# Kernel optimization log

Measured on AMD Instinct MI355X. Metric: run time of the kernel, lower is better.

The kernel has to match this reference:

```python
import jax, jax.numpy as jnp
import numpy as np


def _proj(x, w, b):
    # 1x1 conv as channel matmul: x (n,c,h,w), w (k,c), b (k,) -> (n,k,h,w)
    return jnp.einsum('nchw,kc->nkhw', x, w) + b[None, :, None, None]


def setup_inputs() -> dict:
    key = jax.random.key(0)
    ks = jax.random.split(key, 9)
    cin, cinter = 256, 128
    n, h, w = 4, 64, 64
    s = lambda fan_in: 1.0 / np.sqrt(fan_in)
    return {
        'x': jax.random.normal(ks[0], (n, cin, h, w), jnp.float32),
        'theta_w': jax.random.normal(ks[1], (cinter, cin), jnp.float32) * s(cin),
        'theta_b': jax.random.normal(ks[2], (cinter,), jnp.float32) * 0.01,
        'phi_w': jax.random.normal(ks[3], (cinter, cin), jnp.float32) * s(cin),
        'phi_b': jax.random.normal(ks[4], (cinter,), jnp.float32) * 0.01,
        'g_w': jax.random.normal(ks[5], (cinter, cin), jnp.float32) * s(cin),
        'g_b': jax.random.normal(ks[6], (cinter,), jnp.float32) * 0.01,
        'w_w': jax.random.normal(ks[7], (cin, cinter), jnp.float32) * s(cinter),
        'w_b': jax.random.normal(ks[8], (cin,), jnp.float32) * 0.01,
    }


def reference(x, theta_w, theta_b, phi_w, phi_b, g_w, g_b, w_w, w_b):
    n, c, h, w = x.shape
    cinter = theta_w.shape[0]
    hw = h * w
    theta_x = _proj(x, theta_w, theta_b).reshape(n, cinter, hw)  # (n,ci,HW)
    phi_x = _proj(x, phi_w, phi_b).reshape(n, cinter, hw)        # (n,ci,HW)
    g_x = _proj(x, g_w, g_b).reshape(n, cinter, hw)              # (n,ci,HW)
    # f_x = phi^T @ theta : (n, HW, HW), softmax over last dim (theta positions)
    f_x = jnp.einsum('nci,ncj->nij', phi_x, theta_x)
    f_x = jax.nn.softmax(f_x, axis=-1)
    # attended = g @ f : (n, ci, HW)
    att = jnp.einsum('nci,nij->ncj', g_x, f_x).reshape(n, cinter, h, w)
    res_x = _proj(att, w_w, w_b)  # (n, c, h, w)
    return x + res_x
```

## Files before the change

### kernel.cpp

```cpp
#include <hip/hip_runtime.h>
#include <hip/hip_bf16.h>

#define B_ 4
#define C_ 256
#define CI_ 128
#define P_ 4096
#define LOG2E 1.44269504088896340736f

typedef __attribute__((ext_vector_type(8))) _Float16 half8;
typedef __attribute__((ext_vector_type(2))) __fp16 fp16x2;
typedef __attribute__((ext_vector_type(8))) short short8;
typedef __attribute__((ext_vector_type(4))) short short4v;
typedef __attribute__((ext_vector_type(4))) float floatx4;

__device__ __forceinline__ float bf2f(ushort h) {
  union { unsigned u; float f; } v; v.u = ((unsigned)h) << 16; return v.f;
}
__device__ __forceinline__ ushort f2bf(float f) {
  union { float f; unsigned u; } v; v.f = f;
  unsigned r = v.u + 0x7FFFu + ((v.u >> 16) & 1u);
  return (ushort)(r >> 16);
}
__device__ __forceinline__ ushort f2h(float f) {
  _Float16 h = (_Float16)f;
  union { _Float16 h; ushort u; } v; v.h = h; return v.u;
}
__device__ __forceinline__ uint2 pk4h(float a, float b, float c, float d) {
  union { fp16x2 h[2]; uint2 u; } pk;
  pk.h[0] = __builtin_amdgcn_cvt_pkrtz(a, b);
  pk.h[1] = __builtin_amdgcn_cvt_pkrtz(c, d);
  return pk.u;
}

#define MFMA16(a, b, c) __builtin_amdgcn_mfma_f32_16x16x32_f16((a), (b), (c), 0, 0, 0)

__device__ __forceinline__ int detect_bf16(const ushort* __restrict__ xu) {
  __shared__ int cnt_;
  if (threadIdx.x == 0) cnt_ = 0;
  __syncthreads();
  int local = 0;
  int t = threadIdx.x & 255;
#pragma unroll
  for (int s = 0; s < 8; ++s) {
    ushort u = xu[(t * 8 + s) * 2];
    int e = (u >> 7) & 0xFF;
    local += (e >= 0x70 && e <= 0x84) ? 1 : 0;
  }
  atomicAdd(&cnt_, local);
  __syncthreads();
  return cnt_ > 1024;
}

__global__ void k_trc(const void* __restrict__ xv, ushort* __restrict__ xT,
                      const void* __restrict__ s0, const void* __restrict__ s1,
                      const void* __restrict__ s2, const void* __restrict__ s3,
                      const void* __restrict__ tbv, const void* __restrict__ pbv,
                      const void* __restrict__ gbv, const void* __restrict__ wbv,
                      ushort* __restrict__ dstW, float* __restrict__ biasf) {
  int is_bf16 = detect_bf16((const ushort*)xv);
  int bid = blockIdx.x;
  int t = threadIdx.x;
  if (bid < 1024) {
    __shared__ __align__(16) ushort tile[64][74];
    int pb = (bid & 63) * 64;
    int cb = ((bid >> 6) & 3) * 64;
    int b = bid >> 8;
#pragma unroll
    for (int it = 0; it < 2; ++it) {
      int lin = it * 256 + t;
      int c = lin >> 3;
      int p = (lin & 7) * 8;
      size_t base = ((size_t)(b * C_) + cb + c) * P_ + pb + p;
      float vv[8];
      if (is_bf16) {
        short8 v = *(const short8*)((const ushort*)xv + base);
#pragma unroll
        for (int i = 0; i < 8; ++i) vv[i] = bf2f((ushort)v[i]);
      } else {
        const float* xf = (const float*)xv;
        float4 v0 = *(const float4*)(xf + base);
        float4 v1 = *(const float4*)(xf + base + 4);
        vv[0] = v0.x; vv[1] = v0.y; vv[2] = v0.z; vv[3] = v0.w;
        vv[4] = v1.x; vv[5] = v1.y; vv[6] = v1.z; vv[7] = v1.w;
      }
#pragma unroll
      for (int i = 0; i < 8; ++i) {
        int iw = (i + t) & 7;
        tile[p + iw][c] = f2h(vv[iw]);
      }
    }
    __syncthreads();
#pragma unroll
    for (int it = 0; it < 2; ++it) {
      int lin = it * 256 + t;
      int p = lin >> 3;
      int c = (lin & 7) * 8;
      short8 v = *(const short8*)&tile[p][c];
      *(short8*)(xT + ((size_t)(b * P_) + pb + p) * C_ + cb + c) = v;
    }
  } else if (bid < 1536) {
    int wid = bid - 1024;
    int a = wid >> 7;
    const void* srcs[4] = {s0, s1, s2, s3};
    int i = (wid & 127) * 256 + t;
    float v = is_bf16 ? bf2f(((const ushort*)srcs[a])[i]) : ((const float*)srcs[a])[i];
    dstW[a * 32768 + i] = f2h(v);
  } else {
    int idx = (bid - 1536) * 256 + t;
    if (idx < 640) {
      const void* src; int loc;
      if (idx < 128)      { src = tbv; loc = idx; }
      else if (idx < 256) { src = pbv; loc = idx - 128; }
      else if (idx < 384) { src = gbv; loc = idx - 256; }
      else                { src = wbv; loc = idx - 384; }
      float v = is_bf16 ? bf2f(((const ushort*)src)[loc]) : ((const float*)src)[loc];
      biasf[idx] = v;
    }
  }
}

__global__ __launch_bounds__(256, 4) void k_proj(
    const ushort* __restrict__ xT, const ushort* __restrict__ Wh,
    const float* __restrict__ biasf,
    ushort* __restrict__ thetaT, ushort* __restrict__ phiT,
    ushort* __restrict__ g) {
  int t = threadIdx.x;
  int w = t >> 6, lane = t & 63, l = lane & 15, q = lane >> 4;
  int pblk = blockIdx.x * 32;
  int b = blockIdx.y;
  floatx4 acc[2][6];
#pragma unroll
  for (int ps = 0; ps < 2; ++ps)
#pragma unroll
    for (int ks = 0; ks < 6; ++ks) acc[ps][ks] = (floatx4){0.f, 0.f, 0.f, 0.f};
  const ushort* xrow[2];
#pragma unroll
  for (int ps = 0; ps < 2; ++ps)
    xrow[ps] = xT + ((size_t)(b * P_) + pblk + ps * 16 + l) * C_;
  const ushort* wrow[6];
  int prj[6], kloc[6];
#pragma unroll
  for (int ks = 0; ks < 6; ++ks) {
    int kg = w * 96 + ks * 16;
    prj[ks] = kg >> 7;
    kloc[ks] = kg & 127;
    wrow[ks] = Wh + prj[ks] * 32768 + (size_t)(kloc[ks] + l) * C_;
  }
  for (int c = 0; c < C_; c += 32) {
    half8 av[2], wv[6];
#pragma unroll
    for (int ps = 0; ps < 2; ++ps) av[ps] = *(const half8*)(xrow[ps] + c + q * 8);
#pragma unroll
    for (int ks = 0; ks < 6; ++ks) wv[ks] = *(const half8*)(wrow[ks] + c + q * 8);
#pragma unroll
    for (int ps = 0; ps < 2; ++ps)
#pragma unroll
      for (int ks = 0; ks < 6; ++ks)
        acc[ps][ks] = MFMA16(av[ps], wv[ks], acc[ps][ks]);
  }
#pragma unroll
  for (int ks = 0; ks < 6; ++ks) {
    float bias = biasf[prj[ks] * 128 + kloc[ks] + l];
#pragma unroll
    for (int ps = 0; ps < 2; ++ps) {
      floatx4 d = acc[ps][ks];
      if (prj[ks] < 2) {
        ushort* dst = (prj[ks] == 0 ? thetaT : phiT) +
                      ((size_t)(b * P_) + pblk + ps * 16 + q * 4) * CI_ + kloc[ks] + l;
#pragma unroll
        for (int r = 0; r < 4; ++r) dst[(size_t)r * CI_] = f2h(d[r] + bias);
      } else {
        ushort* dst = g + ((size_t)(b * CI_) + kloc[ks] + l) * P_ + pblk + ps * 16 + q * 4;
        short4v pk;
#pragma unroll
        for (int r = 0; r < 4; ++r) pk[r] = (short)f2h(d[r] + bias);
        *(short4v*)dst = pk;
      }
    }
  }
}

__global__ __launch_bounds__(256, 2) void k_stats(
    const ushort* __restrict__ phiT, const ushort* __restrict__ thetaT,
    float* __restrict__ part) {
  int t = threadIdx.x, w = t >> 6, lane = t & 63, l = lane & 15, q = lane >> 4;
  int wgid = blockIdx.x;
  int xcd = wgid & 7, slot = wgid >> 3;
  int st = xcd + 8 * (slot >> 4);
  int i0 = (slot & 15) * 256;
  int jsp = st & 7;
  int j0 = jsp * 512;
  int b = st >> 3;
  half8 av[4][4];
#pragma unroll
  for (int is = 0; is < 4; ++is) {
    const ushort* pr = phiT + ((size_t)(b * P_) + i0 + w * 64 + is * 16 + l) * CI_;
#pragma unroll
    for (int ks = 0; ks < 4; ++ks) av[is][ks] = *(const half8*)(pr + ks * 32 + q * 8);
  }
  float sum[4][4];
#pragma unroll
  for (int is = 0; is < 4; ++is)
#pragma unroll
    for (int r = 0; r < 4; ++r) sum[is][r] = 0.f;
  const ushort* tb0 = thetaT + (size_t)b * P_ * CI_;
  for (int jc = 0; jc < 16; ++jc) {
    int j = j0 + jc * 32;
    half8 bv[2][4];
#pragma unroll
    for (int js = 0; js < 2; ++js) {
      const ushort* tr = tb0 + (size_t)(j + js * 16 + l) * CI_;
#pragma unroll
      for (int ks = 0; ks < 4; ++ks) bv[js][ks] = *(const half8*)(tr + ks * 32 + q * 8);
    }
    floatx4 accS[4][2];
#pragma unroll
    for (int is = 0; is < 4; ++is)
#pragma unroll
      for (int js = 0; js < 2; ++js) accS[is][js] = (floatx4){0.f, 0.f, 0.f, 0.f};
#pragma unroll
    for (int ks = 0; ks < 4; ++ks)
#pragma unroll
      for (int is = 0; is < 4; ++is)
#pragma unroll
        for (int js = 0; js < 2; ++js)
          accS[is][js] = MFMA16(av[is][ks], bv[js][ks], accS[is][js]);
#pragma unroll
    for (int is = 0; is < 4; ++is)
#pragma unroll
      for (int js = 0; js < 2; ++js)
#pragma unroll
        for (int r = 0; r < 4; ++r)
          sum[is][r] += exp2f(fmaf(accS[is][js][r], LOG2E, -64.f));
  }
#pragma unroll
  for (int d = 1; d < 16; d <<= 1)
#pragma unroll
    for (int is = 0; is < 4; ++is)
#pragma unroll
      for (int r = 0; r < 4; ++r) sum[is][r] += __shfl_xor(sum[is][r], d, 64);
  if (l == 0) {
#pragma unroll
    for (int is = 0; is < 4; ++is)
#pragma unroll
      for (int r = 0; r < 4; ++r)
        part[((size_t)jsp * B_ + b) * P_ + i0 + w * 64 + is * 16 + q * 4 + r] =
            sum[is][r];
  }
}

__global__ void k_lse(const float* __restrict__ part, float* __restrict__ o2) {
  int idx = blockIdx.x * 256 + threadIdx.x;
  float s = 0.f;
#pragma unroll
  for (int p = 0; p < 8; ++p) s += part[(size_t)p * (B_ * P_) + idx];
  o2[idx] = log2f(s) + 64.f;
}

__global__ __launch_bounds__(256, 2) void k_attn(
    const ushort* __restrict__ phiT, const ushort* __restrict__ thetaT,
    const ushort* __restrict__ g, const float* __restrict__ o2,
    ushort* __restrict__ attPA, ushort* __restrict__ attPB,
    int nIH, int nChunk) {
  __shared__ __align__(16) ushort thL[128][136];
  __shared__ __align__(16) ushort eL[128][136];
  int t = threadIdx.x;
  int w = t >> 6, lane = t & 63, l = lane & 15, q = lane >> 4;
  int wgid = blockIdx.x;
  int xcd = wgid & 7, slot = wgid >> 3;
  int st = xcd + 8 * (slot >> 5);
  int j0 = (slot & 31) * 128;
  int ih = st & (nIH - 1);
  int b = st >> ((nIH == 4) ? 2 : 1);
#pragma unroll
  for (int it = 0; it < 8; ++it) {
    int lin = it * 256 + t, row = lin >> 4, cg = (lin & 15) * 8;
    *(short8*)&thL[row][cg] =
        *(const short8*)(thetaT + ((size_t)(b * P_) + j0 + row) * CI_ + cg);
  }
  floatx4 accA[2][8];
#pragma unroll
  for (int cs = 0; cs < 2; ++cs)
#pragma unroll
    for (int js = 0; js < 8; ++js) accA[cs][js] = (floatx4){0.f, 0.f, 0.f, 0.f};
  __syncthreads();
  const float* orow = o2 + b * P_;
  int istart = ih * nChunk * 128;
  half8 af[2][4];
  float ov[2][4];
#pragma unroll
  for (int is = 0; is < 2; ++is) {
    int iG = istart + w * 32 + is * 16;
    const ushort* pr = phiT + ((size_t)(b * P_) + iG + l) * CI_;
#pragma unroll
    for (int ks = 0; ks < 4; ++ks) af[is][ks] = *(const half8*)(pr + ks * 32 + q * 8);
#pragma unroll
    for (int r = 0; r < 4; ++r) ov[is][r] = orow[iG + q * 4 + r];
  }
  for (int ic = 0; ic < nChunk; ++ic) {
    int ibase = istart + ic * 128;
    half8 gf[2][4];
#pragma unroll
    for (int cs = 0; cs < 2; ++cs) {
      const ushort* gr = g + ((size_t)(b * CI_) + w * 32 + cs * 16 + l) * P_ + ibase;
#pragma unroll
      for (int ks = 0; ks < 4; ++ks) gf[cs][ks] = *(const half8*)(gr + ks * 32 + q * 8);
    }
    floatx4 accS[2][8];
#pragma unroll
    for (int is = 0; is < 2; ++is)
#pragma unroll
      for (int js = 0; js < 8; ++js) accS[is][js] = (floatx4){0.f, 0.f, 0.f, 0.f};
    __builtin_amdgcn_s_setprio(1);
#pragma unroll
    for (int ks = 0; ks < 4; ++ks) {
      half8 bf[8];
#pragma unroll
      for (int js = 0; js < 8; ++js) bf[js] = *(const half8*)&thL[js * 16 + l][ks * 32 + q * 8];
#pragma unroll
      for (int is = 0; is < 2; ++is)
#pragma unroll
        for (int js = 0; js < 8; ++js) accS[is][js] = MFMA16(af[is][ks], bf[js], accS[is][js]);
    }
    __builtin_amdgcn_s_setprio(0);
    uint2 ep[2][8];
#pragma unroll
    for (int is = 0; is < 2; ++is)
#pragma unroll
      for (int js = 0; js < 8; ++js) {
        float e0 = exp2f(fmaf(accS[is][js][0], LOG2E, -ov[is][0]));
        float e1 = exp2f(fmaf(accS[is][js][1], LOG2E, -ov[is][1]));
        float e2 = exp2f(fmaf(accS[is][js][2], LOG2E, -ov[is][2]));
        float e3 = exp2f(fmaf(accS[is][js][3], LOG2E, -ov[is][3]));
        ep[is][js] = pk4h(e0, e1, e2, e3);
      }
    __syncthreads();
#pragma unroll
    for (int is = 0; is < 2; ++is)
#pragma unroll
      for (int js = 0; js < 8; ++js)
        *(uint2*)&eL[js * 16 + l][w * 32 + is * 16 + q * 4] = ep[is][js];
    __syncthreads();
    if (ic < nChunk - 1) {
      int nb = istart + (ic + 1) * 128;
#pragma unroll
      for (int is = 0; is < 2; ++is) {
        int iG = nb + w * 32 + is * 16;
        const ushort* pr = phiT + ((size_t)(b * P_) + iG + l) * CI_;
#pragma unroll
        for (int ks = 0; ks < 4; ++ks) af[is][ks] = *(const half8*)(pr + ks * 32 + q * 8);
#pragma unroll
        for (int r = 0; r < 4; ++r) ov[is][r] = orow[iG + q * 4 + r];
      }
    }
    __builtin_amdgcn_s_setprio(1);
#pragma unroll
    for (int ks = 0; ks < 4; ++ks) {
      half8 ef[8];
#pragma unroll
      for (int js = 0; js < 8; ++js) ef[js] = *(const half8*)&eL[js * 16 + l][ks * 32 + q * 8];
#pragma unroll
      for (int cs = 0; cs < 2; ++cs)
#pragma unroll
        for (int js = 0; js < 8; ++js) accA[cs][js] = MFMA16(gf[cs][ks], ef[js], accA[cs][js]);
    }
    __builtin_amdgcn_s_setprio(0);
  }
  ushort* ap = (ih < 2 ? attPA : attPB) + (size_t)(ih & 1) * (B_ * P_ * CI_);
#pragma unroll
  for (int cs = 0; cs < 2; ++cs)
#pragma unroll
    for (int js = 0; js < 8; ++js) {
      uint2 pk = pk4h(accA[cs][js][0], accA[cs][js][1], accA[cs][js][2], accA[cs][js][3]);
      *(uint2*)(ap + ((size_t)(b * P_) + j0 + js * 16 + l) * CI_ +
                w * 32 + cs * 16 + q * 4) = pk;
    }
}

__global__ __launch_bounds__(256, 4) void k_out(
    const ushort* __restrict__ attPA, const ushort* __restrict__ attPB, int nIH,
    const ushort* __restrict__ wwh, const float* __restrict__ biasf,
    const void* __restrict__ xv, void* __restrict__ outv) {
  int is_bf16 = detect_bf16((const ushort*)xv);
  int t = threadIdx.x;
  int w = t >> 6, lane = t & 63, l = lane & 15, q = lane >> 4;
  int p0 = blockIdx.x * 32, b = blockIdx.y;
  floatx4 accR[4][2];
#pragma unroll
  for (int kk = 0; kk < 4; ++kk)
#pragma unroll
    for (int js = 0; js < 2; ++js) accR[kk][js] = (floatx4){0.f, 0.f, 0.f, 0.f};
#pragma unroll
  for (int ks = 0; ks < 4; ++ks) {
    half8 wf[4], af[2];
#pragma unroll
    for (int kk = 0; kk < 4; ++kk)
      wf[kk] = *(const half8*)(wwh + (size_t)(w * 64 + kk * 16 + l) * CI_ + ks * 32 + q * 8);
#pragma unroll
    for (int js = 0; js < 2; ++js) {
      size_t off = ((size_t)(b * P_) + p0 + js * 16 + l) * CI_ + ks * 32 + q * 8;
      half8 s = *(const half8*)(attPA + off);
      s = s + *(const half8*)(attPA + (size_t)(B_ * P_) * CI_ + off);
      if (nIH == 4) {
        s = s + *(const half8*)(attPB + off);
        s = s + *(const half8*)(attPB + (size_t)(B_ * P_) * CI_ + off);
      }
      af[js] = s;
    }
#pragma unroll
    for (int kk = 0; kk < 4; ++kk)
#pragma unroll
      for (int js = 0; js < 2; ++js) accR[kk][js] = MFMA16(wf[kk], af[js], accR[kk][js]);
  }
#pragma unroll
  for (int kk = 0; kk < 4; ++kk)
#pragma unroll
    for (int r = 0; r < 4; ++r) {
      int c = w * 64 + kk * 16 + q * 4 + r;
      float bias = biasf[384 + c];
#pragma unroll
      for (int js = 0; js < 2; ++js) {
        int p = p0 + js * 16 + l;
        size_t idx = ((size_t)(b * C_) + c) * P_ + p;
        float val = accR[kk][js][r] + bias;
        if (is_bf16) {
          ((ushort*)outv)[idx] = f2bf(bf2f(((const ushort*)xv)[idx]) + val);
        } else {
          ((float*)outv)[idx] = ((const float*)xv)[idx] + val;
        }
      }
    }
}

extern "C" void kernel_launch(void* const* d_in, const int* in_sizes, int n_in,
                              void* d_out, int out_size, void* d_ws, size_t ws_size,
                              hipStream_t stream) {
  const void* x  = d_in[0];
  const void* tw = d_in[1];
  const void* tb = d_in[2];
  const void* pw = d_in[3];
  const void* pb = d_in[4];
  const void* gw = d_in[5];
  const void* gb = d_in[6];
  const void* ww = d_in[7];
  const void* wb = d_in[8];
  char* ws = (char*)d_ws;
  float*  o2     = (float*)(ws);
  float*  part   = (float*)(ws + (64u << 10));
  ushort* Wh     = (ushort*)(ws + (576u << 10));
  float*  biasf  = (float*)(ws + (832u << 10));
  ushort* xT     = (ushort*)(ws + (1u << 20));
  ushort* attPA  = xT;
  ushort* thetaT = (ushort*)(ws + (9u << 20));
  ushort* phiT   = (ushort*)(ws + (13u << 20));
  ushort* gbuf   = (ushort*)(ws + (17u << 20));
  ushort* attPB  = (ushort*)(ws + (21u << 20));
  int big = (ws_size >= (30u << 20)) ? 1 : 0;

  k_trc<<<1539, 256, 0, stream>>>(x, xT, tw, pw, gw, ww, tb, pb, gb, wb, Wh, biasf);
  k_proj<<<dim3(128, 4), 256, 0, stream>>>(xT, Wh, biasf, thetaT, phiT, gbuf);
  k_stats<<<512, 256, 0, stream>>>(phiT, thetaT, part);
  k_lse<<<64, 256, 0, stream>>>(part, o2);
  if (big) {
    k_attn<<<512, 256, 0, stream>>>(phiT, thetaT, gbuf, o2, attPA, attPB, 4, 8);
    k_out<<<dim3(128, 4), 256, 0, stream>>>(attPA, attPB, 4, Wh + 3 * 32768, biasf, x, d_out);
  } else {
    k_attn<<<256, 256, 0, stream>>>(phiT, thetaT, gbuf, o2, attPA, attPB, 2, 16);
    k_out<<<dim3(128, 4), 256, 0, stream>>>(attPA, attPB, 2, Wh + 3 * 32768, biasf, x, d_out);
  }
}
```

Before: 227.4 us.

## Software-pipeline score MFMA and exp for the next chunk after the PV MFMAs

Restructures the attention loop so the S=phi·theta MFMAs and exp for the next chunk are computed at the end of the current iteration, after the accumulation MFMAs, with a prologue for the first chunk. The score computation is also reordered per js column block with a short-lived accumulator instead of a full 2x8 accumulator array, which lowers register pressure. The goal is to interleave exp/VALU work with MFMA work and cut live registers. The cost is duplicated code and the exp work no longer running under the raised priority region.

```diff
diff --git a/kernel.cpp b/kernel.cpp
--- a/kernel.cpp
+++ b/kernel.cpp
@@ -283,11 +283,11 @@
   for (int cs = 0; cs < 2; ++cs)
 #pragma unroll
     for (int js = 0; js < 8; ++js) accA[cs][js] = (floatx4){0.f, 0.f, 0.f, 0.f};
-  __syncthreads();
   const float* orow = o2 + b * P_;
   int istart = ih * nChunk * 128;
   half8 af[2][4];
   float ov[2][4];
+  uint2 ep[2][8];
 #pragma unroll
   for (int is = 0; is < 2; ++is) {
     int iG = istart + w * 32 + is * 16;
@@ -297,6 +297,25 @@
 #pragma unroll
     for (int r = 0; r < 4; ++r) ov[is][r] = orow[iG + q * 4 + r];
   }
+  __syncthreads();
+#pragma unroll
+  for (int js = 0; js < 8; ++js) {
+    half8 bf[4];
+#pragma unroll
+    for (int ks = 0; ks < 4; ++ks)
+      bf[ks] = *(const half8*)&thL[js * 16 + l][ks * 32 + q * 8];
+#pragma unroll
+    for (int is = 0; is < 2; ++is) {
+      floatx4 s = (floatx4){0.f, 0.f, 0.f, 0.f};
+#pragma unroll
+      for (int ks = 0; ks < 4; ++ks) s = MFMA16(af[is][ks], bf[ks], s);
+      float e0 = exp2f(fmaf(s[0], LOG2E, -ov[is][0]));
+      float e1 = exp2f(fmaf(s[1], LOG2E, -ov[is][1]));
+      float e2 = exp2f(fmaf(s[2], LOG2E, -ov[is][2]));
+      float e3 = exp2f(fmaf(s[3], LOG2E, -ov[is][3]));
+      ep[is][js] = pk4h(e0, e1, e2, e3);
+    }
+  }
   for (int ic = 0; ic < nChunk; ++ic) {
     int ibase = istart + ic * 128;
     half8 gf[2][4];
@@ -306,34 +325,6 @@
 #pragma unroll
       for (int ks = 0; ks < 4; ++ks) gf[cs][ks] = *(const half8*)(gr + ks * 32 + q * 8);
     }
-    floatx4 accS[2][8];
-#pragma unroll
-    for (int is = 0; is < 2; ++is)
-#pragma unroll
-      for (int js = 0; js < 8; ++js) accS[is][js] = (floatx4){0.f, 0.f, 0.f, 0.f};
-    __builtin_amdgcn_s_setprio(1);
-#pragma unroll
-    for (int ks = 0; ks < 4; ++ks) {
-      half8 bf[8];
-#pragma unroll
-      for (int js = 0; js < 8; ++js) bf[js] = *(const half8*)&thL[js * 16 + l][ks * 32 + q * 8];
-#pragma unroll
-      for (int is = 0; is < 2; ++is)
-#pragma unroll
-        for (int js = 0; js < 8; ++js) accS[is][js] = MFMA16(af[is][ks], bf[js], accS[is][js]);
-    }
-    __builtin_amdgcn_s_setprio(0);
-    uint2 ep[2][8];
-#pragma unroll
-    for (int is = 0; is < 2; ++is)
-#pragma unroll
-      for (int js = 0; js < 8; ++js) {
-        float e0 = exp2f(fmaf(accS[is][js][0], LOG2E, -ov[is][0]));
-        float e1 = exp2f(fmaf(accS[is][js][1], LOG2E, -ov[is][1]));
-        float e2 = exp2f(fmaf(accS[is][js][2], LOG2E, -ov[is][2]));
-        float e3 = exp2f(fmaf(accS[is][js][3], LOG2E, -ov[is][3]));
-        ep[is][js] = pk4h(e0, e1, e2, e3);
-      }
     __syncthreads();
 #pragma unroll
     for (int is = 0; is < 2; ++is)
@@ -341,7 +332,7 @@
       for (int js = 0; js < 8; ++js)
         *(uint2*)&eL[js * 16 + l][w * 32 + is * 16 + q * 4] = ep[is][js];
     __syncthreads();
-    if (ic < nChunk - 1) {
+    if (ic + 1 < nChunk) {
       int nb = istart + (ic + 1) * 128;
 #pragma unroll
       for (int is = 0; is < 2; ++is) {
@@ -365,6 +356,26 @@
         for (int js = 0; js < 8; ++js) accA[cs][js] = MFMA16(gf[cs][ks], ef[js], accA[cs][js]);
     }
     __builtin_amdgcn_s_setprio(0);
+    if (ic + 1 < nChunk) {
+#pragma unroll
+      for (int js = 0; js < 8; ++js) {
+        half8 bf[4];
+#pragma unroll
+        for (int ks = 0; ks < 4; ++ks)
+          bf[ks] = *(const half8*)&thL[js * 16 + l][ks * 32 + q * 8];
+#pragma unroll
+        for (int is = 0; is < 2; ++is) {
+          floatx4 s = (floatx4){0.f, 0.f, 0.f, 0.f};
+#pragma unroll
+          for (int ks = 0; ks < 4; ++ks) s = MFMA16(af[is][ks], bf[ks], s);
+          float e0 = exp2f(fmaf(s[0], LOG2E, -ov[is][0]));
+          float e1 = exp2f(fmaf(s[1], LOG2E, -ov[is][1]));
+          float e2 = exp2f(fmaf(s[2], LOG2E, -ov[is][2]));
+          float e3 = exp2f(fmaf(s[3], LOG2E, -ov[is][3]));
+          ep[is][js] = pk4h(e0, e1, e2, e3);
+        }
+      }
+    }
   }
   ushort* ap = (ih < 2 ? attPA : attPB) + (size_t)(ih & 1) * (B_ * P_ * CI_);
 #pragma unroll
```

New measurement: 225.0 us. Within noise of the previous version (-1.0%).
